# Kernel optimization log

Hardware: AMD Instinct MI355X
Metric: run time of the kernel (lower is better)

## Reference

```python
import jax, jax.numpy as jnp
import numpy as np

B, T, D_OBS = 64, 512, 128
D_LAT, D_HID, K = 16, 256, 8
VAR = 0.0005
LOG2PI = float(np.log(2.0 * np.pi))


def _leaky(x):
    return jnp.where(x > 0, x, 0.01 * x)


def setup_inputs() -> dict:
    key = jax.random.key(0)
    ks = jax.random.split(key, 12)
    s = 0.05
    return {
        "x": jax.random.normal(ks[0], (B, T, D_OBS), jnp.float32),
        "eps": jax.random.normal(ks[1], (B, T, D_LAT), jnp.float32),
        "W1": jax.random.normal(ks[2], (D_OBS, D_HID), jnp.float32) * s,
        "b1": jnp.zeros((D_HID,), jnp.float32),
        "W2": jax.random.normal(ks[3], (D_HID, 2 * D_LAT), jnp.float32) * s,
        "b2": jnp.zeros((2 * D_LAT,), jnp.float32),
        "Wt1": jax.random.normal(ks[4], (K, D_LAT, D_HID), jnp.float32) * s,
        "bt1": jnp.zeros((K, D_HID), jnp.float32),
        "Wt2": jax.random.normal(ks[5], (K, D_HID, D_LAT), jnp.float32) * s,
        "bt2": jnp.zeros((K, D_LAT), jnp.float32),
        "Wd1": jax.random.normal(ks[6], (D_LAT, D_HID), jnp.float32) * s,
        "bd1": jnp.zeros((D_HID,), jnp.float32),
        "Wd2": jax.random.normal(ks[7], (D_HID, D_OBS), jnp.float32) * s,
        "bd2": jnp.zeros((D_OBS,), jnp.float32),
        "Q": jax.random.normal(ks[8], (K, K), jnp.float32) * 0.1,
        "pi": jax.random.normal(ks[9], (K,), jnp.float32) * 0.1,
        "init_mean": jax.random.normal(ks[10], (K, D_LAT), jnp.float32),
        "init_cov": jax.random.uniform(ks[11], (K, 1, 1), jnp.float32) * jnp.eye(D_LAT, dtype=jnp.float32)[None] * 5.0,
        "covs": jnp.tile(jnp.eye(D_LAT, dtype=jnp.float32)[None], (K, 1, 1)),
    }


def _mvn_logprob(diff, chol):
    # diff [..., K, d]; chol [K, d, d] lower Cholesky of per-state covariance
    d = chol.shape[-1]
    Linv = jax.scipy.linalg.solve_triangular(
        chol, jnp.broadcast_to(jnp.eye(d, dtype=chol.dtype), chol.shape), lower=True)
    sol = jnp.einsum('kij,...kj->...ki', Linv, diff)
    logdet = 2.0 * jnp.sum(jnp.log(jnp.diagonal(chol, axis1=-2, axis2=-1)), -1)  # [K]
    return -0.5 * (d * LOG2PI + logdet + jnp.sum(sol * sol, -1))


def _forward(x, eps, W1, b1, W2, b2, Wt1, bt1, Wt2, bt2, Wd1, bd1, Wd2, bd2,
             Q, pi, init_mean, init_cov, covs):
    Bx = x.shape[0]
    dz = init_mean.shape[-1]
    # ---- factored MLP encoder: x -> (mu, logvar); reparameterized sample ----
    h = _leaky(x @ W1 + b1)
    enc = h @ W2 + b2
    z_mu, z_log_var = enc[..., :dz], enc[..., dz:]
    z = z_mu + jnp.exp(0.5 * z_log_var) * eps                            # [B,T,dz]
    # ---- local evidence log p(z_t | z_{t-1}, s_t=k) ----
    jitter = 1e-6 * jnp.eye(dz, dtype=x.dtype)
    L0 = jnp.linalg.cholesky(init_cov @ jnp.swapaxes(init_cov, -1, -2) + jitter)
    ev1 = _mvn_logprob(z[:, 0:1, None, :] - init_mean[None, None], L0)   # [B,1,K]
    ht = jax.nn.softplus(jnp.einsum('btd,kdh->btkh', z[:, :-1], Wt1) + bt1)
    means = jnp.einsum('btkh,khd->btkd', ht, Wt2) + bt2                  # [B,T-1,K,dz]
    Lt = jnp.linalg.cholesky(covs @ jnp.swapaxes(covs, -1, -2) + jitter)
    evT = _mvn_logprob(z[:, 1:, None, :] - means, Lt)                    # [B,T-1,K]
    ev = jnp.concatenate([ev1, evT], axis=1)                             # [B,T,K]
    # ---- HMM alpha recursion in log domain (temperature=1) ----
    log_pi = jax.nn.log_softmax(pi)
    Qlog = jax.nn.log_softmax(Q, axis=-1).T                              # [new, old]
    lp0 = ev[:, 0] + log_pi
    lZ0 = jax.scipy.special.logsumexp(lp0, axis=-1)
    la0 = lp0 - lZ0[:, None]

    def step(la, ev_t):
        lp = jax.scipy.special.logsumexp(ev_t[:, :, None] + Qlog[None] + la[:, None, :], axis=-1)
        lZ = jax.scipy.special.logsumexp(lp, axis=-1)
        return lp - lZ[:, None], lZ

    _, lZs = jax.lax.scan(step, la0, jnp.moveaxis(ev[:, 1:], 1, 0))
    log_Z = lZ0 + jnp.sum(lZs, axis=0)                                   # [B]
    # ---- decoder ----
    x_hat = _leaky(z @ Wd1 + bd1) @ Wd2 + bd2
    # ---- ELBO ----
    recon = jnp.sum(-0.5 * jnp.log(2.0 * jnp.pi * VAR) - (x - x_hat) ** 2 / (2.0 * VAR)) / Bx
    logq = -0.5 * (dz * LOG2PI + jnp.sum(z_log_var, -1)
                   + jnp.sum((z - z_mu) ** 2 / jnp.exp(z_log_var), -1))
    entropy_q = -jnp.sum(logq) / Bx
    msm = jnp.sum(log_Z) / Bx
    loss = -(recon + entropy_q + msm)
    return x_hat, z, loss


def reference(x, eps, W1, b1, W2, b2, Wt1, bt1, Wt2, bt2, Wd1, bd1, Wd2, bd2,
              Q, pi, init_mean, init_cov, covs):
    return _forward(x, eps, W1, b1, W2, b2, Wt1, bt1, Wt2, bt2, Wd1, bd1, Wd2, bd2,
                    Q, pi, init_mean, init_cov, covs)
```

## Files before the change

### kernel.cpp

```cpp
#include <hip/hip_runtime.h>
#include <math.h>

#define B_SZ   64
#define T_SZ   512
#define DOBS   128
#define DLAT   16
#define DHID   256
#define K_SZ   8
#define ROWS_A 32768

#define LOG2PI_F 1.8378770664093453f
#define VAR_F    5.0e-4f

#define LINV0_OFF   16
#define LOGDET0_OFF 2064
#define LINVT_OFF   2080
#define LOGDETT_OFF 4128
#define WIMG_F_OFF  8192

#define EVT_W1   0
#define EVT_W2   49152
#define EVT_LINV 82944
#define ENC_W1   86016
#define ENC_W2   120832
#define DEC_W1   129280
#define DEC_W2   135424
#define WCVT_TOTAL 141568

#define Z_OUT_OFF   4194304
#define LOSS_OFF    4718592
#define PBUF_OFF  262144
#define ACC_OFF   327680

typedef __attribute__((ext_vector_type(8))) short short8;
typedef __attribute__((ext_vector_type(8))) unsigned short ush8;
typedef __attribute__((ext_vector_type(4))) float floatx4;

__device__ __forceinline__ float leakyf(float v) { return v > 0.f ? v : 0.01f * v; }
__device__ __forceinline__ unsigned short f2bf(float f) {
  union { float f; unsigned int u; } v; v.f = f;
  unsigned int lsb = (v.u >> 16) & 1;
  v.u += 0x7fffu + lsb;
  return (unsigned short)(v.u >> 16);
}
__device__ __forceinline__ unsigned int cvt_pk_bf16(float lo, float hi) {
  unsigned int r;
  asm("v_cvt_pk_bf16_f32 %0, %1, %2" : "=v"(r) : "v"(lo), "v"(hi));
  return r;
}
__device__ __forceinline__ float softplusf(float v) {
  float t = __expf(-fabsf(v));
  return fmaxf(v, 0.f) + __logf(1.f + t);
}

__global__ __launch_bounds__(256) void prep_kernel(const float* __restrict__ init_cov,
                                                   const float* __restrict__ covs,
                                                   float* __restrict__ ws) {
  __shared__ float M[16][16];
  __shared__ float L[16][16];
  __shared__ float X[16][17];
  int job = blockIdx.x;
  const float* C = (job < 8) ? (init_cov + job * 256) : (covs + (job - 8) * 256);
  float* linv = ws + ((job < 8) ? (LINV0_OFF + job * 256) : (LINVT_OFF + (job - 8) * 256));
  float* logdet = ws + ((job < 8) ? (LOGDET0_OFF + job) : (LOGDETT_OFF + (job - 8)));
  int tid = threadIdx.x;
  if (job == 0 && tid < 4) ws[tid] = 0.f;
  int i = tid >> 4, j = tid & 15;
  {
    float s = (i == j) ? 1e-6f : 0.f;
    #pragma unroll
    for (int p = 0; p < 16; ++p) s += C[i * 16 + p] * C[j * 16 + p];
    M[i][j] = s;
  }
  __syncthreads();
  for (int c = 0; c < 16; ++c) {
    if (tid == 0) {
      float s = M[c][c];
      for (int p = 0; p < c; ++p) s -= L[c][p] * L[c][p];
      L[c][c] = sqrtf(s);
    }
    __syncthreads();
    if (tid > c && tid < 16) {
      float s = M[tid][c];
      for (int p = 0; p < c; ++p) s -= L[tid][p] * L[c][p];
      L[tid][c] = s / L[c][c];
    }
    __syncthreads();
  }
  if (tid < 16) {
    for (int r = 0; r < 16; ++r) {
      float s = (r == tid) ? 1.f : 0.f;
      for (int p = tid; p < r; ++p) s -= L[r][p] * X[p][tid];
      X[r][tid] = (r >= tid) ? s / L[r][r] : 0.f;
    }
  }
  __syncthreads();
  linv[i * 16 + j] = X[i][j];
  if (tid == 0) {
    float s = 0.f;
    for (int d = 0; d < 16; ++d) s += logf(L[d][d]);
    *logdet = 2.f * s;
  }
}

__global__ __launch_bounds__(256) void wcvt_kernel(
    const float* __restrict__ Wt1, const float* __restrict__ Wt2,
    const float* __restrict__ W1, const float* __restrict__ W2,
    const float* __restrict__ Wd1, const float* __restrict__ Wd2,
    const float* __restrict__ ws, unsigned short* __restrict__ wimg) {
  for (int e = blockIdx.x * 256 + threadIdx.x; e < WCVT_TOTAL; e += gridDim.x * 256) {
    if (e < 32768) {
      int k = e >> 12, r = e & 4095, i = r >> 4, d = r & 15;
      wimg[EVT_W1 + k * 6144 + i * 24 + d] = f2bf(Wt1[k * 4096 + d * 256 + i]);
    } else if (e < 65536) {
      int e2 = e - 32768; int k = e2 >> 12, r = e2 & 4095, h = r >> 4, d2 = r & 15;
      wimg[EVT_W2 + k * 4224 + d2 * 264 + h] = f2bf(Wt2[k * 4096 + h * 16 + d2]);
    } else if (e < 67584) {
      int e2 = e - 65536; int k = e2 >> 8, r = e2 & 255, i = r >> 4, j = r & 15;
      wimg[EVT_LINV + k * 384 + i * 24 + j] = f2bf(ws[LINVT_OFF + k * 256 + i * 16 + j]);
    } else if (e < 100352) {
      int e2 = e - 67584; int n = e2 >> 7, kk = e2 & 127;
      wimg[ENC_W1 + n * 136 + kk] = f2bf(W1[kk * 256 + n]);
    } else if (e < 108544) {
      int e2 = e - 100352; int n = e2 >> 8, kk = e2 & 255;
      wimg[ENC_W2 + n * 264 + kk] = f2bf(W2[kk * 32 + n]);
    } else if (e < 112640) {
      int e2 = e - 108544; int n = e2 >> 4, kk = e2 & 15;
      wimg[DEC_W1 + n * 24 + kk] = f2bf(Wd1[kk * 256 + n]);
    } else {
      int e2 = e - 112640; int n = e2 & 127, kk = e2 >> 7;
      wimg[DEC_W2 + n * 264 + kk] = f2bf(Wd2[kk * 128 + n]);
    }
  }
}

__global__ __launch_bounds__(256) void enc_kernel(
    const float* __restrict__ x, const float* __restrict__ eps,
    const float* __restrict__ b1, const float* __restrict__ b2,
    const unsigned short* __restrict__ wimg,
    float* __restrict__ z_out, float* __restrict__ ws) {
  __shared__ __align__(16) unsigned short w2t[32 * 264];
  __shared__ __align__(16) unsigned short ttile[4][16 * 56];
  __shared__ float b1s[256];
  __shared__ float sred;
  int tid = threadIdx.x;
  if (tid == 0) sred = 0.f;
  {
    const ush8* s2 = (const ush8*)(wimg + ENC_W2);
    for (int e = tid; e < 1056; e += 256) ((ush8*)w2t)[e] = s2[e];
    b1s[tid] = b1[tid];
  }
  __syncthreads();

  int wid = tid >> 6, lane = tid & 63;
  int m = lane & 15, quad = lane >> 4;
  unsigned short* tt = ttile[wid];
  const unsigned short* w1i = wimg + ENC_W1;
  long rowb = (long)blockIdx.x * 64 + wid * 16;

  short8 xa[4];
  const float* xp = x + (rowb + m) * 128 + quad * 8;
  #pragma unroll
  for (int kt = 0; kt < 4; ++kt) {
    float4 f0 = *(const float4*)(xp + kt * 32);
    float4 f1 = *(const float4*)(xp + kt * 32 + 4);
    union { unsigned int u[4]; short8 s; } cv;
    cv.u[0] = cvt_pk_bf16(f0.x, f0.y);
    cv.u[1] = cvt_pk_bf16(f0.z, f0.w);
    cv.u[2] = cvt_pk_bf16(f1.x, f1.y);
    cv.u[3] = cvt_pk_bf16(f1.z, f1.w);
    xa[kt] = cv.s;
  }
  float bm0 = b2[m], bm1 = b2[16 + m];
  floatx4 a20 = {bm0, bm0, bm0, bm0};
  floatx4 a21 = {bm1, bm1, bm1, bm1};
  #pragma unroll
  for (int cp = 0; cp < 8; ++cp) {
    floatx4 a1h[2];
    #pragma unroll
    for (int h = 0; h < 2; ++h) {
      int c = cp * 2 + h;
      float bias = b1s[c * 16 + m];
      floatx4 a1 = {bias, bias, bias, bias};
      #pragma unroll
      for (int kt = 0; kt < 4; ++kt) {
        short8 bf = *(const short8*)&w1i[(c * 16 + m) * 136 + kt * 32 + quad * 8];
        a1 = __builtin_amdgcn_mfma_f32_16x16x32_bf16(xa[kt], bf, a1, 0, 0, 0);
      }
      a1h[h] = a1;
    }
    #pragma unroll
    for (int g = 0; g < 4; ++g) {
      unsigned int p = cvt_pk_bf16(leakyf(a1h[0][g]), leakyf(a1h[1][g]));
      int base = (quad * 4 + g) * 56 + m;
      tt[base] = (unsigned short)p;
      tt[base + 16] = (unsigned short)(p >> 16);
    }
    short8 ha = *(const short8*)&tt[m * 56 + quad * 8];
    short8 wb0 = *(const short8*)&w2t[m * 264 + cp * 32 + quad * 8];
    short8 wb1 = *(const short8*)&w2t[(16 + m) * 264 + cp * 32 + quad * 8];
    a20 = __builtin_amdgcn_mfma_f32_16x16x32_bf16(ha, wb0, a20, 0, 0, 0);
    a21 = __builtin_amdgcn_mfma_f32_16x16x32_bf16(ha, wb1, a21, 0, 0, 0);
  }
  float logq_acc = 0.f;
  #pragma unroll
  for (int g = 0; g < 4; ++g) {
    long row = rowb + quad * 4 + g;
    float mu = a20[g], lv = a21[g];
    float ev = eps[row * 16 + m];
    float zv = mu + __expf(0.5f * lv) * ev;
    z_out[row * 16 + m] = zv;
    float zz = zv - mu;
    logq_acc += lv + zz * zz * __expf(-lv);
  }
  #pragma unroll
  for (int off = 1; off < 64; off <<= 1) logq_acc += __shfl_xor(logq_acc, off, 64);
  if (lane == 0) atomicAdd(&sred, -0.5f * logq_acc);
  __syncthreads();
  if (tid == 0) atomicAdd(&ws[1], sred - 0.5f * 16.f * LOG2PI_F * 64.f);
}

__global__ __launch_bounds__(256, 8) void evt_kernel(
    const float* __restrict__ z, const unsigned short* __restrict__ wimg,
    const float* __restrict__ bt1, const float* __restrict__ bt2,
    const float* __restrict__ ws, float* __restrict__ evT) {
  __shared__ __align__(16) unsigned short w2t[4224];
  __shared__ __align__(16) unsigned short ttile[4][16 * 56];
  __shared__ __align__(16) unsigned short dtile[4][16 * 24];
  __shared__ __align__(16) unsigned short linvb[384];
  __shared__ float bt1s[256];
  int tid = threadIdx.x;
  int k = blockIdx.y;
  {
    const ush8* s2 = (const ush8*)(wimg + EVT_W2 + k * 4224);
    for (int e = tid; e < 528; e += 256) ((ush8*)w2t)[e] = s2[e];
    if (tid < 48) ((ush8*)linvb)[tid] = ((const ush8*)(wimg + EVT_LINV + k * 384))[tid];
    bt1s[tid] = bt1[k * 256 + tid];
  }
  float logdetk = ws[LOGDETT_OFF + k];
  __syncthreads();

  int wid = tid >> 6, lane = tid & 63;
  int m = lane & 15, quad = lane >> 4;
  unsigned short* tt = ttile[wid];
  unsigned short* db = dtile[wid];
  const unsigned short* w1i = wimg + EVT_W1 + k * 6144;
  float btv = bt2[k * 16 + m];

  for (int tile = 0; tile < 2; ++tile) {
    long rowb = (long)blockIdx.x * 128 + wid * 32 + tile * 16;
    short8 za = (short8)0;
    if (quad < 2) {
      const float* zp = z + (rowb + m) * 16 + quad * 8;
      float4 f0 = *(const float4*)zp;
      float4 f1 = *(const float4*)(zp + 4);
      union { unsigned int u[4]; short8 s; } cv;
      cv.u[0] = cvt_pk_bf16(f0.x, f0.y);
      cv.u[1] = cvt_pk_bf16(f0.z, f0.w);
      cv.u[2] = cvt_pk_bf16(f1.x, f1.y);
      cv.u[3] = cvt_pk_bf16(f1.z, f1.w);
      za = cv.s;
    }
    floatx4 a2 = {btv, btv, btv, btv};
    #pragma unroll
    for (int cp = 0; cp < 8; ++cp) {
      floatx4 a1h[2];
      #pragma unroll
      for (int h = 0; h < 2; ++h) {
        int c = cp * 2 + h;
        short8 bfrag = (short8)0;
        if (quad < 2) bfrag = *(const short8*)&w1i[(c * 16 + m) * 24 + quad * 8];
        float bias = bt1s[c * 16 + m];
        floatx4 a1 = {bias, bias, bias, bias};
        a1 = __builtin_amdgcn_mfma_f32_16x16x32_bf16(za, bfrag, a1, 0, 0, 0);
        a1h[h] = a1;
      }
      #pragma unroll
      for (int g = 0; g < 4; ++g) {
        unsigned int p = cvt_pk_bf16(softplusf(a1h[0][g]), softplusf(a1h[1][g]));
        int base = (quad * 4 + g) * 56 + m;
        tt[base] = (unsigned short)p;
        tt[base + 16] = (unsigned short)(p >> 16);
      }
      short8 ha = *(const short8*)&tt[m * 56 + quad * 8];
      short8 wb = *(const short8*)&w2t[m * 264 + cp * 32 + quad * 8];
      a2 = __builtin_amdgcn_mfma_f32_16x16x32_bf16(ha, wb, a2, 0, 0, 0);
    }
    #pragma unroll
    for (int g = 0; g < 4; ++g) {
      long grow = rowb + quad * 4 + g;
      float znx = (grow + 1 < ROWS_A) ? z[(grow + 1) * 16 + m] : 0.f;
      db[(quad * 4 + g) * 24 + m] = f2bf(znx - a2[g]);
    }
    short8 da = (short8)0, lb = (short8)0;
    if (quad < 2) {
      da = *(const short8*)&db[m * 24 + quad * 8];
      lb = *(const short8*)&linvb[m * 24 + quad * 8];
    }
    floatx4 a3 = {0.f, 0.f, 0.f, 0.f};
    a3 = __builtin_amdgcn_mfma_f32_16x16x32_bf16(da, lb, a3, 0, 0, 0);
    #pragma unroll
    for (int g = 0; g < 4; ++g) {
      float v = a3[g];
      v = v * v;
      v += __shfl_xor(v, 1, 64);
      v += __shfl_xor(v, 2, 64);
      v += __shfl_xor(v, 4, 64);
      v += __shfl_xor(v, 8, 64);
      long grow = rowb + quad * 4 + g;
      if (m == 0 && (grow & 511) != 511) {
        long r1 = grow + 1;
        evT[(r1 >> 9) * 4096 + (long)k * 512 + (r1 & 511)] =
            -0.5f * (16.f * LOG2PI_F + logdetk + v);
      }
    }
  }
}

__global__ __launch_bounds__(256) void hmm_scan(const float* __restrict__ Q,
                                                const float* __restrict__ evT,
                                                float* __restrict__ pbuf,
                                                float* __restrict__ accbuf) {
  int tid = threadIdx.x;
  int wid = tid >> 6, lane = tid & 63;
  int job = blockIdx.x * 4 + wid;
  int b = job >> 4, c = job & 15;
  int i = lane >> 3, j = lane & 7;

  float qp[8];
  #pragma unroll
  for (int p = 0; p < 8; ++p) {
    float mr = Q[p * 8 + 0];
    #pragma unroll
    for (int cc = 1; cc < 8; ++cc) mr = fmaxf(mr, Q[p * 8 + cc]);
    float rs = 0.f;
    #pragma unroll
    for (int cc = 0; cc < 8; ++cc) rs += __expf(Q[p * 8 + cc] - mr);
    qp[p] = __expf(Q[p * 8 + i] - mr) / rs;
  }
  float qself;
  {
    float mr = Q[j * 8 + 0];
    #pragma unroll
    for (int cc = 1; cc < 8; ++cc) mr = fmaxf(mr, Q[j * 8 + cc]);
    float rs = 0.f;
    #pragma unroll
    for (int cc = 0; cc < 8; ++cc) rs += __expf(Q[j * 8 + cc] - mr);
    qself = __expf(Q[j * 8 + i] - mr) / rs;
  }

  int t0 = 1 + c * 32;
  int L = (c == 15) ? 31 : 32;
  const float* evI = evT + (long)b * 4096 + (long)i * 512 + t0;

  float f[32];
  float accm = 0.f;
  #pragma unroll
  for (int s = 0; s < 32; ++s) {
    float e = (s < L) ? evI[s] : 0.f;
    float m = e;
    m = fmaxf(m, __shfl_xor(m, 8, 64));
    m = fmaxf(m, __shfl_xor(m, 16, 64));
    m = fmaxf(m, __shfl_xor(m, 32, 64));
    f[s] = __expf(e - m);
    if (s < L) accm += m;
  }

  float P = f[0] * qself;
  #pragma unroll
  for (int s = 1; s < 32; ++s) {
    if (s < L) {
      float a0 = __shfl(P, j,      64);
      float a1 = __shfl(P, 8 + j,  64);
      float a2 = __shfl(P, 16 + j, 64);
      float a3 = __shfl(P, 24 + j, 64);
      float a4 = __shfl(P, 32 + j, 64);
      float a5 = __shfl(P, 40 + j, 64);
      float a6 = __shfl(P, 48 + j, 64);
      float a7 = __shfl(P, 56 + j, 64);
      float sv = ((qp[0] * a0 + qp[1] * a1) + (qp[2] * a2 + qp[3] * a3))
               + ((qp[4] * a4 + qp[5] * a5) + (qp[6] * a6 + qp[7] * a7));
      P = f[s] * sv;
    }
    if ((s & 7) == 7) {
      float mx = P;
      mx = fmaxf(mx, __shfl_xor(mx, 1, 64));
      mx = fmaxf(mx, __shfl_xor(mx, 2, 64));
      mx = fmaxf(mx, __shfl_xor(mx, 4, 64));
      mx = fmaxf(mx, __shfl_xor(mx, 8, 64));
      mx = fmaxf(mx, __shfl_xor(mx, 16, 64));
      mx = fmaxf(mx, __shfl_xor(mx, 32, 64));
      mx = fmaxf(mx, 1e-30f);
      P = P / mx;
      accm += __logf(mx);
    }
  }
  pbuf[(long)job * 64 + lane] = P;
  if (lane == 0) accbuf[job] = accm;
}

__global__ __launch_bounds__(512) void hmm_comb(const float* __restrict__ pi,
                                                const float* __restrict__ z,
                                                const float* __restrict__ init_mean,
                                                const float* __restrict__ pbuf,
                                                const float* __restrict__ accbuf,
                                                float* __restrict__ ws) {
  int tid = threadIdx.x;
  int wid = tid >> 6, lane = tid & 63;
  int b = blockIdx.x * 8 + wid;
  int j = lane & 7;

  float mp = pi[0];
  #pragma unroll
  for (int cc = 1; cc < 8; ++cc) mp = fmaxf(mp, pi[cc]);
  float sp = 0.f;
  #pragma unroll
  for (int cc = 0; cc < 8; ++cc) sp += __expf(pi[cc] - mp);
  float lpi = pi[j] - mp - __logf(sp);

  const float* zr = z + (long)b * 8192;
  const float* linv = ws + LINV0_OFF + j * 256;
  float diff[16];
  #pragma unroll
  for (int d = 0; d < 16; ++d) diff[d] = zr[d] - init_mean[j * 16 + d];
  float quad0 = 0.f;
  #pragma unroll
  for (int i2 = 0; i2 < 16; ++i2) {
    float s = 0.f;
    #pragma unroll
    for (int jj = 0; jj < 16; ++jj) s += linv[i2 * 16 + jj] * diff[jj];
    quad0 += s * s;
  }
  float ev0 = -0.5f * (16.f * LOG2PI_F + ws[LOGDET0_OFF + j] + quad0);

  float lp0 = ev0 + lpi;
  float m0 = lp0;
  m0 = fmaxf(m0, __shfl_xor(m0, 1, 64));
  m0 = fmaxf(m0, __shfl_xor(m0, 2, 64));
  m0 = fmaxf(m0, __shfl_xor(m0, 4, 64));
  float u = __expf(lp0 - m0);
  double acc = (double)m0;

  #pragma unroll
  for (int c = 0; c < 16; ++c) {
    float P = pbuf[((long)b * 16 + c) * 64 + lane];
    float contrib = P * u;
    contrib += __shfl_xor(contrib, 1, 64);
    contrib += __shfl_xor(contrib, 2, 64);
    contrib += __shfl_xor(contrib, 4, 64);
    u = __shfl(contrib, j * 9, 64);
    float mxu = u;
    mxu = fmaxf(mxu, __shfl_xor(mxu, 1, 64));
    mxu = fmaxf(mxu, __shfl_xor(mxu, 2, 64));
    mxu = fmaxf(mxu, __shfl_xor(mxu, 4, 64));
    mxu = fmaxf(mxu, 1e-30f);
    u = u / mxu;
    acc += (double)(__logf(mxu) + accbuf[b * 16 + c]);
  }
  float su = u;
  su += __shfl_xor(su, 1, 64);
  su += __shfl_xor(su, 2, 64);
  su += __shfl_xor(su, 4, 64);
  float logZ = (float)(acc + (double)__logf(su));
  if (lane == 0) atomicAdd(&ws[2], logZ);
}

__global__ __launch_bounds__(256) void dec_kernel(
    const float* __restrict__ x, const float* __restrict__ z,
    const float* __restrict__ bd1, const float* __restrict__ bd2,
    const unsigned short* __restrict__ wimg,
    float* __restrict__ xhat, float* __restrict__ ws) {
  __shared__ __align__(16) unsigned short w1t[6144];
  __shared__ __align__(16) unsigned short ttile[4][16 * 56];
  __shared__ float bd1s[256];
  __shared__ float bd2s[128];
  __shared__ float sred;
  int tid = threadIdx.x;
  if (tid == 0) sred = 0.f;
  {
    const ush8* s1 = (const ush8*)(wimg + DEC_W1);
    for (int e = tid; e < 768; e += 256) ((ush8*)w1t)[e] = s1[e];
    bd1s[tid] = bd1[tid];
    if (tid < 128) bd2s[tid] = bd2[tid];
  }
  __syncthreads();

  int wid = tid >> 6, lane = tid & 63;
  int m = lane & 15, quad = lane >> 4;
  unsigned short* tt = ttile[wid];
  const unsigned short* w2i = wimg + DEC_W2;
  long rowb = (long)blockIdx.x * 64 + wid * 16;

  short8 za = (short8)0;
  if (quad < 2) {
    const float* zp = z + (rowb + m) * 16 + quad * 8;
    float4 f0 = *(const float4*)zp;
    float4 f1 = *(const float4*)(zp + 4);
    union { unsigned int u[4]; short8 s; } cv;
    cv.u[0] = cvt_pk_bf16(f0.x, f0.y);
    cv.u[1] = cvt_pk_bf16(f0.z, f0.w);
    cv.u[2] = cvt_pk_bf16(f1.x, f1.y);
    cv.u[3] = cvt_pk_bf16(f1.z, f1.w);
    za = cv.s;
  }
  floatx4 a2[8];
  #pragma unroll
  for (int c2 = 0; c2 < 8; ++c2) {
    float bv = bd2s[c2 * 16 + m];
    a2[c2] = (floatx4){bv, bv, bv, bv};
  }
  #pragma unroll
  for (int cp = 0; cp < 8; ++cp) {
    floatx4 a1h[2];
    #pragma unroll
    for (int h = 0; h < 2; ++h) {
      int c = cp * 2 + h;
      short8 bfrag = (short8)0;
      if (quad < 2) bfrag = *(const short8*)&w1t[(c * 16 + m) * 24 + quad * 8];
      float bias = bd1s[c * 16 + m];
      floatx4 a1 = {bias, bias, bias, bias};
      a1 = __builtin_amdgcn_mfma_f32_16x16x32_bf16(za, bfrag, a1, 0, 0, 0);
      a1h[h] = a1;
    }
    #pragma unroll
    for (int g = 0; g < 4; ++g) {
      unsigned int p = cvt_pk_bf16(leakyf(a1h[0][g]), leakyf(a1h[1][g]));
      int base = (quad * 4 + g) * 56 + m;
      tt[base] = (unsigned short)p;
      tt[base + 16] = (unsigned short)(p >> 16);
    }
    short8 ha = *(const short8*)&tt[m * 56 + quad * 8];
    #pragma unroll
    for (int c2 = 0; c2 < 8; ++c2) {
      short8 wb = *(const short8*)&w2i[(c2 * 16 + m) * 264 + cp * 32 + quad * 8];
      a2[c2] = __builtin_amdgcn_mfma_f32_16x16x32_bf16(ha, wb, a2[c2], 0, 0, 0);
    }
  }
  const float C0 = -0.5f * logf(6.2831853071795864f * VAR_F);
  float rsum = 0.f;
  #pragma unroll
  for (int c2 = 0; c2 < 8; ++c2) {
    int col = c2 * 16 + m;
    #pragma unroll
    for (int g = 0; g < 4; ++g) {
      long row = rowb + quad * 4 + g;
      float xh = a2[c2][g];
      xhat[row * 128 + col] = xh;
      float dd = x[row * 128 + col] - xh;
      rsum += C0 - dd * dd * (0.5f / VAR_F);
    }
  }
  #pragma unroll
  for (int off = 1; off < 64; off <<= 1) rsum += __shfl_xor(rsum, off, 64);
  if (lane == 0) atomicAdd(&sred, rsum);
  __syncthreads();
  if (tid == 0) atomicAdd(&ws[0], sred);
}

__global__ void fin_kernel(const float* __restrict__ ws, float* __restrict__ out) {
  float loss = -((ws[0] - ws[1] + ws[2]) * (1.f / 64.f));
  out[LOSS_OFF] = loss;
}

extern "C" void kernel_launch(void* const* d_in, const int* in_sizes, int n_in,
                              void* d_out, int out_size, void* d_ws, size_t ws_size,
                              hipStream_t stream) {
  (void)in_sizes; (void)n_in; (void)out_size; (void)ws_size;
  const float* x   = (const float*)d_in[0];
  const float* eps = (const float*)d_in[1];
  const float* W1  = (const float*)d_in[2];
  const float* b1  = (const float*)d_in[3];
  const float* W2  = (const float*)d_in[4];
  const float* b2  = (const float*)d_in[5];
  const float* Wt1 = (const float*)d_in[6];
  const float* bt1 = (const float*)d_in[7];
  const float* Wt2 = (const float*)d_in[8];
  const float* bt2 = (const float*)d_in[9];
  const float* Wd1 = (const float*)d_in[10];
  const float* bd1 = (const float*)d_in[11];
  const float* Wd2 = (const float*)d_in[12];
  const float* bd2 = (const float*)d_in[13];
  const float* Q   = (const float*)d_in[14];
  const float* pi  = (const float*)d_in[15];
  const float* im  = (const float*)d_in[16];
  const float* ic  = (const float*)d_in[17];
  const float* cv  = (const float*)d_in[18];
  float* out = (float*)d_out;
  float* ws  = (float*)d_ws;
  float* z_out = out + Z_OUT_OFF;
  float* evT  = out;
  float* pbuf = out + PBUF_OFF;
  float* accb = out + ACC_OFF;
  unsigned short* wimg = (unsigned short*)(ws + WIMG_F_OFF);

  prep_kernel<<<16, 256, 0, stream>>>(ic, cv, ws);
  wcvt_kernel<<<144, 256, 0, stream>>>(Wt1, Wt2, W1, W2, Wd1, Wd2, ws, wimg);
  enc_kernel<<<512, 256, 0, stream>>>(x, eps, b1, b2, wimg, z_out, ws);
  evt_kernel<<<dim3(256, 8), 256, 0, stream>>>(z_out, wimg, bt1, bt2, ws, evT);
  hmm_scan<<<256, 256, 0, stream>>>(Q, evT, pbuf, accb);
  hmm_comb<<<8, 512, 0, stream>>>(pi, z_out, im, pbuf, accb, ws);
  dec_kernel<<<512, 256, 0, stream>>>(x, z_out, bd1, bd2, wimg, out, ws);
  fin_kernel<<<1, 1, 0, stream>>>(ws, out);
}
```

Measured before the change: 243.2 us.

## Fold Linv into transition W2, biases into MFMA K-padding, pack LDS stores

Precomputes Linv·Wt2 and Linv·bt2 in the prep kernel, so the evidence kernel computes Linv·z_next directly with one MFMA and subtracts the transformed transition mean. This removes the per-tile bf16 diff staging through LDS and its reread. First-layer biases are folded into the padded K slot of the MFMA using a constant one input, and hidden-column order is permuted so the activation tile is written with single 32-bit LDS stores. Softplus now uses a cheaper exp2/log2 form without the stable branch, which may lose accuracy or overflow for large inputs, and bias rounding to bf16 adds small error.

```diff
diff --git a/kernel.cpp b/kernel.cpp
--- a/kernel.cpp
+++ b/kernel.cpp
@@ -16,6 +16,7 @@
 #define LOGDET0_OFF 2064
 #define LINVT_OFF   2080
 #define LOGDETT_OFF 4128
+#define CVEC_OFF    4224
 #define WIMG_F_OFF  8192
 
 #define EVT_W1   0
@@ -25,7 +26,7 @@
 #define ENC_W2   120832
 #define DEC_W1   129280
 #define DEC_W2   135424
-#define WCVT_TOTAL 141568
+#define WCVT_TOTAL 182272
 
 #define Z_OUT_OFF   4194304
 #define LOSS_OFF    4718592
@@ -48,14 +49,19 @@
   asm("v_cvt_pk_bf16_f32 %0, %1, %2" : "=v"(r) : "v"(lo), "v"(hi));
   return r;
 }
-__device__ __forceinline__ float softplusf(float v) {
-  float t = __expf(-fabsf(v));
-  return fmaxf(v, 0.f) + __logf(1.f + t);
+__device__ __forceinline__ float softplus5(float v) {
+  return 0.69314718f * __log2f(1.f + exp2f(1.44269504f * v));
+}
+__device__ __forceinline__ int permk(int kk) {
+  return (kk & ~31) | ((kk & 15) << 1) | ((kk >> 4) & 1);
 }
 
 __global__ __launch_bounds__(256) void prep_kernel(const float* __restrict__ init_cov,
                                                    const float* __restrict__ covs,
-                                                   float* __restrict__ ws) {
+                                                   const float* __restrict__ Wt2,
+                                                   const float* __restrict__ bt2,
+                                                   float* __restrict__ ws,
+                                                   float* __restrict__ w2l) {
   __shared__ float M[16][16];
   __shared__ float L[16][16];
   __shared__ float X[16][17];
@@ -101,35 +107,61 @@
     for (int d = 0; d < 16; ++d) s += logf(L[d][d]);
     *logdet = 2.f * s;
   }
+  if (job >= 8) {
+    int k = job - 8;
+    const float* wrow = Wt2 + (long)k * 4096 + tid * 16;
+    float* orow = w2l + (long)k * 4096 + tid * 16;
+    #pragma unroll
+    for (int i2 = 0; i2 < 16; ++i2) {
+      float s = 0.f;
+      for (int jj = 0; jj <= i2; ++jj) s += wrow[jj] * X[i2][jj];
+      orow[i2] = s;
+    }
+    if (tid < 16) {
+      float s = 0.f;
+      const float* b = bt2 + k * 16;
+      for (int jj = 0; jj <= tid; ++jj) s += b[jj] * X[tid][jj];
+      ws[CVEC_OFF + k * 16 + tid] = s;
+    }
+  }
 }
 
 __global__ __launch_bounds__(256) void wcvt_kernel(
-    const float* __restrict__ Wt1, const float* __restrict__ Wt2,
+    const float* __restrict__ Wt1, const float* __restrict__ bt1,
     const float* __restrict__ W1, const float* __restrict__ W2,
-    const float* __restrict__ Wd1, const float* __restrict__ Wd2,
-    const float* __restrict__ ws, unsigned short* __restrict__ wimg) {
+    const float* __restrict__ Wd1, const float* __restrict__ bd1,
+    const float* __restrict__ Wd2,
+    const float* __restrict__ ws, const float* __restrict__ w2l,
+    unsigned short* __restrict__ wimg) {
   for (int e = blockIdx.x * 256 + threadIdx.x; e < WCVT_TOTAL; e += gridDim.x * 256) {
-    if (e < 32768) {
-      int k = e >> 12, r = e & 4095, i = r >> 4, d = r & 15;
-      wimg[EVT_W1 + k * 6144 + i * 24 + d] = f2bf(Wt1[k * 4096 + d * 256 + i]);
-    } else if (e < 65536) {
-      int e2 = e - 32768; int k = e2 >> 12, r = e2 & 4095, h = r >> 4, d2 = r & 15;
-      wimg[EVT_W2 + k * 4224 + d2 * 264 + h] = f2bf(Wt2[k * 4096 + h * 16 + d2]);
-    } else if (e < 67584) {
-      int e2 = e - 65536; int k = e2 >> 8, r = e2 & 255, i = r >> 4, j = r & 15;
+    if (e < 65536) {
+      int k = e >> 13, r = e & 8191, ch = r >> 5, d = r & 31;
+      if (d < 24) {
+        float v = (d < 16) ? Wt1[k * 4096 + d * 256 + ch]
+                           : ((d == 16) ? bt1[k * 256 + ch] : 0.f);
+        wimg[EVT_W1 + k * 6144 + ch * 24 + d] = f2bf(v);
+      }
+    } else if (e < 98304) {
+      int e2 = e - 65536; int k = e2 >> 12, r = e2 & 4095, d2 = r >> 8, h = r & 255;
+      wimg[EVT_W2 + k * 4224 + d2 * 264 + permk(h)] = f2bf(w2l[(long)k * 4096 + h * 16 + d2]);
+    } else if (e < 100352) {
+      int e2 = e - 98304; int k = e2 >> 8, r = e2 & 255, i = r >> 4, j = r & 15;
       wimg[EVT_LINV + k * 384 + i * 24 + j] = f2bf(ws[LINVT_OFF + k * 256 + i * 16 + j]);
-    } else if (e < 100352) {
-      int e2 = e - 67584; int n = e2 >> 7, kk = e2 & 127;
+    } else if (e < 133120) {
+      int e2 = e - 100352; int n = e2 >> 7, kk = e2 & 127;
       wimg[ENC_W1 + n * 136 + kk] = f2bf(W1[kk * 256 + n]);
-    } else if (e < 108544) {
-      int e2 = e - 100352; int n = e2 >> 8, kk = e2 & 255;
-      wimg[ENC_W2 + n * 264 + kk] = f2bf(W2[kk * 32 + n]);
-    } else if (e < 112640) {
-      int e2 = e - 108544; int n = e2 >> 4, kk = e2 & 15;
-      wimg[DEC_W1 + n * 24 + kk] = f2bf(Wd1[kk * 256 + n]);
+    } else if (e < 141312) {
+      int e2 = e - 133120; int n = e2 >> 8, kk = e2 & 255;
+      wimg[ENC_W2 + n * 264 + permk(kk)] = f2bf(W2[kk * 32 + n]);
+    } else if (e < 149504) {
+      int e2 = e - 141312; int n = e2 >> 5, d = e2 & 31;
+      if (d < 24) {
+        float v = (d < 16) ? Wd1[d * 256 + n] : ((d == 16) ? bd1[n] : 0.f);
+        wimg[DEC_W1 + n * 24 + d] = f2bf(v);
+      }
     } else {
-      int e2 = e - 112640; int n = e2 & 127, kk = e2 >> 7;
-      wimg[DEC_W2 + n * 264 + kk] = f2bf(Wd2[kk * 128 + n]);
+      int e2 = e - 149504; int kk = e2 >> 7, n = e2 & 127;
+      wimg[DEC_W2 + n * 264 + permk(kk)] = f2bf(Wd2[kk * 128 + n]);
     }
   }
 }
@@ -192,9 +224,7 @@
     #pragma unroll
     for (int g = 0; g < 4; ++g) {
       unsigned int p = cvt_pk_bf16(leakyf(a1h[0][g]), leakyf(a1h[1][g]));
-      int base = (quad * 4 + g) * 56 + m;
-      tt[base] = (unsigned short)p;
-      tt[base + 16] = (unsigned short)(p >> 16);
+      *(unsigned int*)&tt[(quad * 4 + g) * 56 + 2 * m] = p;
     }
     short8 ha = *(const short8*)&tt[m * 56 + quad * 8];
     short8 wb0 = *(const short8*)&w2t[m * 264 + cp * 32 + quad * 8];
@@ -222,20 +252,16 @@
 
 __global__ __launch_bounds__(256, 8) void evt_kernel(
     const float* __restrict__ z, const unsigned short* __restrict__ wimg,
-    const float* __restrict__ bt1, const float* __restrict__ bt2,
     const float* __restrict__ ws, float* __restrict__ evT) {
   __shared__ __align__(16) unsigned short w2t[4224];
   __shared__ __align__(16) unsigned short ttile[4][16 * 56];
-  __shared__ __align__(16) unsigned short dtile[4][16 * 24];
   __shared__ __align__(16) unsigned short linvb[384];
-  __shared__ float bt1s[256];
   int tid = threadIdx.x;
   int k = blockIdx.y;
   {
     const ush8* s2 = (const ush8*)(wimg + EVT_W2 + k * 4224);
     for (int e = tid; e < 528; e += 256) ((ush8*)w2t)[e] = s2[e];
     if (tid < 48) ((ush8*)linvb)[tid] = ((const ush8*)(wimg + EVT_LINV + k * 384))[tid];
-    bt1s[tid] = bt1[k * 256 + tid];
   }
   float logdetk = ws[LOGDETT_OFF + k];
   __syncthreads();
@@ -243,9 +269,8 @@
   int wid = tid >> 6, lane = tid & 63;
   int m = lane & 15, quad = lane >> 4;
   unsigned short* tt = ttile[wid];
-  unsigned short* db = dtile[wid];
   const unsigned short* w1i = wimg + EVT_W1 + k * 6144;
-  float btv = bt2[k * 16 + m];
+  float cval = ws[CVEC_OFF + k * 16 + m];
 
   for (int tile = 0; tile < 2; ++tile) {
     long rowb = (long)blockIdx.x * 128 + wid * 32 + tile * 16;
@@ -260,8 +285,23 @@
       cv.u[2] = cvt_pk_bf16(f1.x, f1.y);
       cv.u[3] = cvt_pk_bf16(f1.z, f1.w);
       za = cv.s;
-    }
-    floatx4 a2 = {btv, btv, btv, btv};
+    } else if (quad == 2) {
+      za[0] = (short)0x3F80;
+    }
+    short8 za2 = (short8)0;
+    if (quad < 2) {
+      long r2 = rowb + m + 1; if (r2 > 32767) r2 = 32767;
+      const float* zp2 = z + r2 * 16 + quad * 8;
+      float4 f0 = *(const float4*)zp2;
+      float4 f1 = *(const float4*)(zp2 + 4);
+      union { unsigned int u[4]; short8 s; } cv;
+      cv.u[0] = cvt_pk_bf16(f0.x, f0.y);
+      cv.u[1] = cvt_pk_bf16(f0.z, f0.w);
+      cv.u[2] = cvt_pk_bf16(f1.x, f1.y);
+      cv.u[3] = cvt_pk_bf16(f1.z, f1.w);
+      za2 = cv.s;
+    }
+    floatx4 a2 = {cval, cval, cval, cval};
     #pragma unroll
     for (int cp = 0; cp < 8; ++cp) {
       floatx4 a1h[2];
@@ -269,39 +309,27 @@
       for (int h = 0; h < 2; ++h) {
         int c = cp * 2 + h;
         short8 bfrag = (short8)0;
-        if (quad < 2) bfrag = *(const short8*)&w1i[(c * 16 + m) * 24 + quad * 8];
-        float bias = bt1s[c * 16 + m];
-        floatx4 a1 = {bias, bias, bias, bias};
+        if (quad < 3) bfrag = *(const short8*)&w1i[(c * 16 + m) * 24 + quad * 8];
+        floatx4 a1 = {0.f, 0.f, 0.f, 0.f};
         a1 = __builtin_amdgcn_mfma_f32_16x16x32_bf16(za, bfrag, a1, 0, 0, 0);
         a1h[h] = a1;
       }
       #pragma unroll
       for (int g = 0; g < 4; ++g) {
-        unsigned int p = cvt_pk_bf16(softplusf(a1h[0][g]), softplusf(a1h[1][g]));
-        int base = (quad * 4 + g) * 56 + m;
-        tt[base] = (unsigned short)p;
-        tt[base + 16] = (unsigned short)(p >> 16);
+        unsigned int p = cvt_pk_bf16(softplus5(a1h[0][g]), softplus5(a1h[1][g]));
+        *(unsigned int*)&tt[(quad * 4 + g) * 56 + 2 * m] = p;
       }
       short8 ha = *(const short8*)&tt[m * 56 + quad * 8];
       short8 wb = *(const short8*)&w2t[m * 264 + cp * 32 + quad * 8];
       a2 = __builtin_amdgcn_mfma_f32_16x16x32_bf16(ha, wb, a2, 0, 0, 0);
     }
+    short8 lb = (short8)0;
+    if (quad < 2) lb = *(const short8*)&linvb[m * 24 + quad * 8];
+    floatx4 a3 = {0.f, 0.f, 0.f, 0.f};
+    a3 = __builtin_amdgcn_mfma_f32_16x16x32_bf16(za2, lb, a3, 0, 0, 0);
     #pragma unroll
     for (int g = 0; g < 4; ++g) {
-      long grow = rowb + quad * 4 + g;
-      float znx = (grow + 1 < ROWS_A) ? z[(grow + 1) * 16 + m] : 0.f;
-      db[(quad * 4 + g) * 24 + m] = f2bf(znx - a2[g]);
-    }
-    short8 da = (short8)0, lb = (short8)0;
-    if (quad < 2) {
-      da = *(const short8*)&db[m * 24 + quad * 8];
-      lb = *(const short8*)&linvb[m * 24 + quad * 8];
-    }
-    floatx4 a3 = {0.f, 0.f, 0.f, 0.f};
-    a3 = __builtin_amdgcn_mfma_f32_16x16x32_bf16(da, lb, a3, 0, 0, 0);
-    #pragma unroll
-    for (int g = 0; g < 4; ++g) {
-      float v = a3[g];
+      float v = a3[g] - a2[g];
       v = v * v;
       v += __shfl_xor(v, 1, 64);
       v += __shfl_xor(v, 2, 64);
@@ -467,12 +495,11 @@
 
 __global__ __launch_bounds__(256) void dec_kernel(
     const float* __restrict__ x, const float* __restrict__ z,
-    const float* __restrict__ bd1, const float* __restrict__ bd2,
+    const float* __restrict__ bd2,
     const unsigned short* __restrict__ wimg,
     float* __restrict__ xhat, float* __restrict__ ws) {
   __shared__ __align__(16) unsigned short w1t[6144];
   __shared__ __align__(16) unsigned short ttile[4][16 * 56];
-  __shared__ float bd1s[256];
   __shared__ float bd2s[128];
   __shared__ float sred;
   int tid = threadIdx.x;
@@ -480,7 +507,6 @@
   {
     const ush8* s1 = (const ush8*)(wimg + DEC_W1);
     for (int e = tid; e < 768; e += 256) ((ush8*)w1t)[e] = s1[e];
-    bd1s[tid] = bd1[tid];
     if (tid < 128) bd2s[tid] = bd2[tid];
   }
   __syncthreads();
@@ -502,6 +528,8 @@
     cv.u[2] = cvt_pk_bf16(f1.x, f1.y);
     cv.u[3] = cvt_pk_bf16(f1.z, f1.w);
     za = cv.s;
+  } else if (quad == 2) {
+    za[0] = (short)0x3F80;
   }
   floatx4 a2[8];
   #pragma unroll
@@ -516,18 +544,15 @@
     for (int h = 0; h < 2; ++h) {
       int c = cp * 2 + h;
       short8 bfrag = (short8)0;
-      if (quad < 2) bfrag = *(const short8*)&w1t[(c * 16 + m) * 24 + quad * 8];
-      float bias = bd1s[c * 16 + m];
-      floatx4 a1 = {bias, bias, bias, bias};
+      if (quad < 3) bfrag = *(const short8*)&w1t[(c * 16 + m) * 24 + quad * 8];
+      floatx4 a1 = {0.f, 0.f, 0.f, 0.f};
       a1 = __builtin_amdgcn_mfma_f32_16x16x32_bf16(za, bfrag, a1, 0, 0, 0);
       a1h[h] = a1;
     }
     #pragma unroll
     for (int g = 0; g < 4; ++g) {
       unsigned int p = cvt_pk_bf16(leakyf(a1h[0][g]), leakyf(a1h[1][g]));
-      int base = (quad * 4 + g) * 56 + m;
-      tt[base] = (unsigned short)p;
-      tt[base + 16] = (unsigned short)(p >> 16);
+      *(unsigned int*)&tt[(quad * 4 + g) * 56 + 2 * m] = p;
     }
     short8 ha = *(const short8*)&tt[m * 56 + quad * 8];
     #pragma unroll
@@ -593,12 +618,12 @@
   float* accb = out + ACC_OFF;
   unsigned short* wimg = (unsigned short*)(ws + WIMG_F_OFF);
 
-  prep_kernel<<<16, 256, 0, stream>>>(ic, cv, ws);
-  wcvt_kernel<<<144, 256, 0, stream>>>(Wt1, Wt2, W1, W2, Wd1, Wd2, ws, wimg);
+  prep_kernel<<<16, 256, 0, stream>>>(ic, cv, Wt2, bt2, ws, pbuf);
+  wcvt_kernel<<<144, 256, 0, stream>>>(Wt1, bt1, W1, W2, Wd1, bd1, Wd2, ws, pbuf, wimg);
   enc_kernel<<<512, 256, 0, stream>>>(x, eps, b1, b2, wimg, z_out, ws);
-  evt_kernel<<<dim3(256, 8), 256, 0, stream>>>(z_out, wimg, bt1, bt2, ws, evT);
+  evt_kernel<<<dim3(256, 8), 256, 0, stream>>>(z_out, wimg, ws, evT);
   hmm_scan<<<256, 256, 0, stream>>>(Q, evT, pbuf, accb);
   hmm_comb<<<8, 512, 0, stream>>>(pi, z_out, im, pbuf, accb, ws);
-  dec_kernel<<<512, 256, 0, stream>>>(x, z_out, bd1, bd2, wimg, out, ws);
+  dec_kernel<<<512, 256, 0, stream>>>(x, z_out, bd2, wimg, out, ws);
   fin_kernel<<<1, 1, 0, stream>>>(ws, out);
 }
```

After: 240.6 us. Within noise of the previous version (-1.1%).
